# Kernel optimization log

Measured on AMD Instinct MI355X. Metric: run time of the kernel, lower is better.

The kernel has to match this reference:

```python
import jax, jax.numpy as jnp
import numpy as np

N = 50000
E = 800000
F_IN = 128
CONV_OUT = 128
CONV_LAYERS = 2
LSTM_OUT = 128
OUT_CH = 64


def setup_inputs() -> dict:
    key = jax.random.key(0)
    ks = jax.random.split(key, 16)
    s = 0.05
    inp = {
        "x": jax.random.normal(ks[0], (N, F_IN), jnp.float32),
        "edge_index": jax.random.randint(ks[1], (2, E), 0, N, dtype=jnp.int32),
        "edge_weight": jax.random.uniform(ks[2], (E,), jnp.float32),
        "H": jax.random.normal(ks[3], (1, N, LSTM_OUT), jnp.float32),
        "C": jax.random.normal(ks[4], (1, N, LSTM_OUT), jnp.float32),
        # GatedGraphConv params
        "ggc_weight": jax.random.normal(ks[5], (CONV_LAYERS, CONV_OUT, CONV_OUT), jnp.float32) * s,
        "gru_wih": jax.random.normal(ks[6], (3 * CONV_OUT, CONV_OUT), jnp.float32) * s,
        "gru_whh": jax.random.normal(ks[7], (3 * CONV_OUT, CONV_OUT), jnp.float32) * s,
        "gru_bih": jax.random.normal(ks[8], (3 * CONV_OUT,), jnp.float32) * s,
        "gru_bhh": jax.random.normal(ks[9], (3 * CONV_OUT,), jnp.float32) * s,
        # LSTM params (single layer, gate order i,f,g,o as in torch)
        "lstm_wih": jax.random.normal(ks[10], (4 * LSTM_OUT, CONV_OUT), jnp.float32) * s,
        "lstm_whh": jax.random.normal(ks[11], (4 * LSTM_OUT, LSTM_OUT), jnp.float32) * s,
        "lstm_bih": jax.random.normal(ks[12], (4 * LSTM_OUT,), jnp.float32) * s,
        "lstm_bhh": jax.random.normal(ks[13], (4 * LSTM_OUT,), jnp.float32) * s,
        # output linear
        "lin_w": jax.random.normal(ks[14], (OUT_CH, LSTM_OUT), jnp.float32) * s,
        "lin_b": jax.random.normal(ks[15], (OUT_CH,), jnp.float32) * s,
    }
    return inp


def reference(x, edge_index, edge_weight, H, C, ggc_weight, gru_wih, gru_whh,
              gru_bih, gru_bhh, lstm_wih, lstm_whh, lstm_bih, lstm_bhh, lin_w, lin_b):
    n = x.shape[0]
    out_dim = ggc_weight.shape[1]
    # GatedGraphConv: zero-pad input features up to out_dim if needed
    if x.shape[1] < out_dim:
        h = jnp.pad(x, ((0, 0), (0, out_dim - x.shape[1])))
    else:
        h = x
    src, dst = edge_index[0], edge_index[1]
    for i in range(ggc_weight.shape[0]):
        m = h @ ggc_weight[i]                      # [N, out]
        msg = m[src] * edge_weight[:, None]        # gather + weight, [E, out]
        agg = jax.ops.segment_sum(msg, dst, num_segments=n)  # scatter-add
        # GRUCell(input=agg, hidden=h)
        gi = agg @ gru_wih.T + gru_bih
        gh = h @ gru_whh.T + gru_bhh
        i_r, i_z, i_n = jnp.split(gi, 3, axis=-1)
        h_r, h_z, h_n = jnp.split(gh, 3, axis=-1)
        r = jax.nn.sigmoid(i_r + h_r)
        z = jax.nn.sigmoid(i_z + h_z)
        ncand = jnp.tanh(i_n + r * h_n)
        h = (1.0 - z) * ncand + z * h
    # single-timestep, single-layer LSTM (torch gate order i,f,g,o)
    hx, cx = H[0], C[0]
    gates = h @ lstm_wih.T + lstm_bih + hx @ lstm_whh.T + lstm_bhh
    ig, fg, gg, og = jnp.split(gates, 4, axis=-1)
    ig = jax.nn.sigmoid(ig)
    fg = jax.nn.sigmoid(fg)
    gg = jnp.tanh(gg)
    og = jax.nn.sigmoid(og)
    c_new = fg * cx + ig * gg
    h_new = og * jnp.tanh(c_new)
    out = jax.nn.relu(h_new) @ lin_w.T + lin_b     # relu then linear head
    return (out, h_new[None], c_new[None])
```

## Files before the change

### kernel.cpp

```cpp
#include <hip/hip_runtime.h>
#include <math.h>

#define N_NODES 50000
#define E_EDGES 800000
#define KD 128
#define NBLK_SCAN 196
#define RT_TILES 3125
#define CELL_RB 128
#define CELL_STRIDE (CELL_RB * 4)
#define CELL_BLOCKS 1024
#define NBUCKETS 196
#define FB_CHUNK 3125

typedef __attribute__((ext_vector_type(8))) short bf16x8;
typedef __attribute__((ext_vector_type(4))) float f32x4;

__device__ __forceinline__ float fsig(float x) { return 1.f / (1.f + __expf(-x)); }
__device__ __forceinline__ float ftanh(float x) { return 1.f - 2.f / (1.f + __expf(2.f * x)); }

__device__ __forceinline__ unsigned short f2bf(float f) {
    unsigned u = __float_as_uint(f);
    return (unsigned short)((u + 0x7FFFu + ((u >> 16) & 1u)) >> 16);
}
__device__ __forceinline__ float bf2f(unsigned short b) {
    return __uint_as_float(((unsigned)b) << 16);
}
__device__ __forceinline__ bf16x8 ldfrag(const unsigned short* p) {
    return *(const bf16x8*)(const void*)p;
}
__device__ __forceinline__ void stage_frag(const unsigned short* g, unsigned short* l) {
    __builtin_amdgcn_global_load_lds(
        (const __attribute__((address_space(1))) unsigned int*)g,
        (__attribute__((address_space(3))) unsigned int*)l, 16, 0, 0);
}
__device__ __forceinline__ void cell_decode(int id, int& x, int& y) {
    y = ((id >> 6) << 3) + (id & 7);
    x = (id >> 3) & 7;
}

#define PB_XH 12500
#define PB_W  12684
#define PB_F  13068
#define PB_CD 16193
__global__ __launch_bounds__(256) void prologue(
        const float* __restrict__ x, const float* __restrict__ H,
        const float* __restrict__ gru_whh, const float* __restrict__ lstm_wih,
        const float* __restrict__ lstm_whh, const float* __restrict__ lin_w,
        const float* __restrict__ ggc_w, const float* __restrict__ gru_wih,
        const int* __restrict__ ei,
        unsigned short* __restrict__ hb, unsigned short* __restrict__ Hxb,
        unsigned short* __restrict__ whhb, unsigned short* __restrict__ lwihb,
        unsigned short* __restrict__ lwhhb, unsigned short* __restrict__ linwb,
        unsigned short* __restrict__ WfT, int* __restrict__ deg) {
    const int b = blockIdx.x;
    if (b < PB_XH) {
        int t = b * 256 + threadIdx.x;
        const int n4 = N_NODES * KD / 4;
        const float* in; unsigned short* out; int idx;
        if (t < n4) { in = x; out = hb; idx = t; }
        else { in = H; out = Hxb; idx = t - n4; }
        float4 v = ((const float4*)in)[idx];
        ushort4 o;
        o.x = f2bf(v.x); o.y = f2bf(v.y); o.z = f2bf(v.z); o.w = f2bf(v.w);
        ((ushort4*)out)[idx] = o;
    } else if (b < PB_W) {
        int t = (b - PB_XH) * 256 + threadIdx.x;
        const float* in; unsigned short* out; int idx;
        if      (t < 12288)  { in = gru_whh;  out = whhb;  idx = t; }
        else if (t < 28672)  { in = lstm_wih; out = lwihb; idx = t - 12288; }
        else if (t < 45056)  { in = lstm_whh; out = lwhhb; idx = t - 28672; }
        else if (t < 47104)  { in = lin_w;    out = linwb; idx = t - 45056; }
        else return;
        float4 v = ((const float4*)in)[idx];
        ushort4 o;
        o.x = f2bf(v.x); o.y = f2bf(v.y); o.z = f2bf(v.z); o.w = f2bf(v.w);
        ((ushort4*)out)[idx] = o;
    } else if (b < PB_F) {
        int j = b - PB_W;
        __shared__ float wi[128];
        int k = threadIdx.x & 127;
        int l = threadIdx.x >> 7;
        if (threadIdx.x < 128) wi[k] = gru_wih[j * 128 + k];
        __syncthreads();
        const float* wg = ggc_w + l * 16384 + k * 128;
        float s = 0.f;
#pragma unroll 8
        for (int c = 0; c < 128; c += 4) {
            float4 a = *(const float4*)(wg + c);
            s += a.x * wi[c] + a.y * wi[c + 1] + a.z * wi[c + 2] + a.w * wi[c + 3];
        }
        WfT[((size_t)l * 384 + j) * 128 + k] = f2bf(s);
    } else {
        int e = (b - PB_F) * 256 + threadIdx.x;
        if (e < E_EDGES) atomicAdd(&deg[ei[E_EDGES + e]], 1);
    }
}

__global__ __launch_bounds__(256) void scan_p1(const int* __restrict__ deg,
                                               int* __restrict__ excl,
                                               int* __restrict__ bsum) {
    __shared__ int part[256];
    const int t = threadIdx.x;
    const int i = blockIdx.x * 256 + t;
    int v = (i < N_NODES) ? deg[i] : 0;
    part[t] = v;
    __syncthreads();
#pragma unroll
    for (int off = 1; off < 256; off <<= 1) {
        int u = (t >= off) ? part[t - off] : 0;
        __syncthreads();
        part[t] += u;
        __syncthreads();
    }
    if (i < N_NODES) excl[i] = part[t] - v;
    if (t == 255) bsum[blockIdx.x] = part[255];
}

__global__ __launch_bounds__(256) void scan_p2(int* __restrict__ bsum,
                                               int* __restrict__ rowptrN) {
    __shared__ int part[256];
    const int t = threadIdx.x;
    int v = (t < NBLK_SCAN) ? bsum[t] : 0;
    part[t] = v;
    __syncthreads();
#pragma unroll
    for (int off = 1; off < 256; off <<= 1) {
        int u = (t >= off) ? part[t - off] : 0;
        __syncthreads();
        part[t] += u;
        __syncthreads();
    }
    if (t < NBLK_SCAN) bsum[t] = part[t] - v;
    if (t == 255) *rowptrN = part[255];
}

__global__ __launch_bounds__(256) void scan_p3(const int* __restrict__ bsum,
                                               int* __restrict__ rowptr,
                                               int* __restrict__ bucketCur) {
    int i = blockIdx.x * 256 + threadIdx.x;
    if (i >= N_NODES) return;
    int r = rowptr[i] + bsum[blockIdx.x];
    rowptr[i] = r;
    if ((i & 255) == 0) bucketCur[i >> 8] = r;
}

__global__ __launch_bounds__(256) void fill_bucket(const int* __restrict__ ei,
                                                   const float* __restrict__ ew,
                                                   int* __restrict__ bucketCur,
                                                   int2* __restrict__ stage_sw,
                                                   int* __restrict__ stage_dst) {
    __shared__ int hist[NBUCKETS];
    __shared__ int base[NBUCKETS];
    __shared__ int loff[NBUCKETS];
    const int t = threadIdx.x;
    const int e0 = blockIdx.x * FB_CHUNK;
    const int e1 = min(e0 + FB_CHUNK, E_EDGES);
    for (int i = t; i < NBUCKETS; i += 256) { hist[i] = 0; loff[i] = 0; }
    __syncthreads();
    for (int e = e0 + t; e < e1; e += 256)
        atomicAdd(&hist[ei[E_EDGES + e] >> 8], 1);
    __syncthreads();
    for (int i = t; i < NBUCKETS; i += 256)
        base[i] = hist[i] ? atomicAdd(&bucketCur[i], hist[i]) : 0;
    __syncthreads();
    for (int e = e0 + t; e < e1; e += 256) {
        int dst = ei[E_EDGES + e];
        int bk = dst >> 8;
        int pos = base[bk] + atomicAdd(&loff[bk], 1);
        int2 pk;
        pk.x = ei[e];
        pk.y = __float_as_int(ew[e]);
        stage_sw[pos] = pk;
        stage_dst[pos] = dst;
    }
}

__global__ __launch_bounds__(256) void fill_final(const int* __restrict__ rowptr,
                                                  const int2* __restrict__ stage_sw,
                                                  const int* __restrict__ stage_dst,
                                                  int2* __restrict__ sEdge) {
    __shared__ int rbase[256];
    __shared__ int cnt[256];
    __shared__ int e1s;
    const int b = blockIdx.x;
    const int t = threadIdx.x;
    const int node0 = b << 8;
    const int nn = min(256, N_NODES - node0);
    if (t < nn) rbase[t] = rowptr[node0 + t];
    cnt[t] = 0;
    if (t == 0) e1s = rowptr[min(node0 + 256, N_NODES)];
    __syncthreads();
    const int e0 = rbase[0];
    const int e1 = e1s;
    for (int e = e0 + t; e < e1; e += 256) {
        int dl = stage_dst[e] & 255;
        int pos = rbase[dl] + atomicAdd(&cnt[dl], 1);
        sEdge[pos] = stage_sw[e];
    }
}

__global__ __launch_bounds__(256) void gather_agg_bf16(const unsigned short* __restrict__ m,
                                                       const int* __restrict__ rowptr,
                                                       const int2* __restrict__ sEdge,
                                                       unsigned short* __restrict__ agg) {
    int wid = (blockIdx.x * 256 + threadIdx.x) >> 6;
    if (wid >= N_NODES) return;
    int lane = threadIdx.x & 63;
    int q = lane >> 4, li = lane & 15;
    int f0 = li << 3;
    int e0 = rowptr[wid], e1 = rowptr[wid + 1];
    float acc[8] = {0.f, 0.f, 0.f, 0.f, 0.f, 0.f, 0.f, 0.f};
    int e = e0 + q;
    bf16x8 v = {0, 0, 0, 0, 0, 0, 0, 0};
    float w0 = 0.f;
    if (e < e1) {
        int2 pk0 = sEdge[e];
        w0 = __int_as_float(pk0.y);
        v = ldfrag(m + (size_t)pk0.x * KD + f0);
    }
    int2 pk1 = make_int2(0, 0);
    if (e + 4 < e1) pk1 = sEdge[e + 4];
    for (; e < e1; e += 4) {
        float wc = w0;
        bf16x8 vc = v;
        if (e + 4 < e1) {
            w0 = __int_as_float(pk1.y);
            v = ldfrag(m + (size_t)pk1.x * KD + f0);
        }
        if (e + 8 < e1) pk1 = sEdge[e + 8];
#pragma unroll
        for (int j = 0; j < 8; ++j)
            acc[j] += wc * bf2f((unsigned short)vc[j]);
    }
#pragma unroll
    for (int j = 0; j < 8; ++j) {
        acc[j] += __shfl_xor(acc[j], 16, 64);
        acc[j] += __shfl_xor(acc[j], 32, 64);
    }
    if (q == 0) {
        bf16x8 o;
#pragma unroll
        for (int j = 0; j < 8; ++j) o[j] = (short)f2bf(acc[j]);
        *(bf16x8*)(agg + (size_t)wid * KD + f0) = o;
    }
}

__global__ __launch_bounds__(256) void gru_fused(const unsigned short* __restrict__ Agg,
                                                 const unsigned short* __restrict__ Hin,
                                                 unsigned short* __restrict__ Hout,
                                                 const unsigned short* __restrict__ Wih,
                                                 const unsigned short* __restrict__ Whh,
                                                 const float* __restrict__ bih,
                                                 const float* __restrict__ bhh) {
    int cg, rb;
    cell_decode(blockIdx.x, cg, rb);
    __shared__ unsigned short lds[24 * 512];
    const int lane = threadIdx.x & 63, wave = threadIdx.x >> 6;
    const int rl = lane & 15, kg = lane >> 4;
    const int col0 = cg * 16;
    for (int q = wave; q < 24; q += 4) {
        int s = q >> 2, kk = q & 3;
        const unsigned short* src = (s < 3 ? Wih + (size_t)s * 128 * KD
                                           : Whh + (size_t)(s - 3) * 128 * KD)
                                    + (size_t)(col0 + rl) * KD + kk * 32 + kg * 8;
        stage_frag(src, lds + q * 512);
    }
    __syncthreads();
    const int col = col0 + rl;
    const float b_ir = bih[col], b_iz = bih[128 + col], b_in = bih[256 + col];
    const float b_hr = bhh[col], b_hz = bhh[128 + col], b_hn = bhh[256 + col];
    int rt = rb * 4 + wave;
    if (rt >= RT_TILES) return;
    bf16x8 a1[4], a2[4];
    unsigned short hvc[4];
#pragma unroll
    for (int kk = 0; kk < 4; ++kk) {
        a1[kk] = ldfrag(Agg + ((size_t)rt * 16 + rl) * KD + kk * 32 + kg * 8);
        a2[kk] = ldfrag(Hin + ((size_t)rt * 16 + rl) * KD + kk * 32 + kg * 8);
    }
#pragma unroll
    for (int p = 0; p < 4; ++p)
        hvc[p] = Hin[(size_t)(rt * 16 + kg * 4 + p) * KD + col];
    while (rt < RT_TILES) {
        const int rtn = rt + CELL_STRIDE;
        bf16x8 n1[4], n2[4];
        unsigned short hvn[4];
        if (rtn < RT_TILES) {
#pragma unroll
            for (int kk = 0; kk < 4; ++kk) {
                n1[kk] = ldfrag(Agg + ((size_t)rtn * 16 + rl) * KD + kk * 32 + kg * 8);
                n2[kk] = ldfrag(Hin + ((size_t)rtn * 16 + rl) * KD + kk * 32 + kg * 8);
            }
#pragma unroll
            for (int p = 0; p < 4; ++p)
                hvn[p] = Hin[(size_t)(rtn * 16 + kg * 4 + p) * KD + col];
        }
        f32x4 ir = {0.f,0.f,0.f,0.f}, iz = ir, in_ = ir, hr = ir, hz = ir, hn = ir;
#pragma unroll
        for (int kk = 0; kk < 4; ++kk) {
            ir  = __builtin_amdgcn_mfma_f32_16x16x32_bf16(a1[kk], ldfrag(lds + (0*4+kk)*512 + lane*8), ir,  0, 0, 0);
            iz  = __builtin_amdgcn_mfma_f32_16x16x32_bf16(a1[kk], ldfrag(lds + (1*4+kk)*512 + lane*8), iz,  0, 0, 0);
            in_ = __builtin_amdgcn_mfma_f32_16x16x32_bf16(a1[kk], ldfrag(lds + (2*4+kk)*512 + lane*8), in_, 0, 0, 0);
            hr  = __builtin_amdgcn_mfma_f32_16x16x32_bf16(a2[kk], ldfrag(lds + (3*4+kk)*512 + lane*8), hr,  0, 0, 0);
            hz  = __builtin_amdgcn_mfma_f32_16x16x32_bf16(a2[kk], ldfrag(lds + (4*4+kk)*512 + lane*8), hz,  0, 0, 0);
            hn  = __builtin_amdgcn_mfma_f32_16x16x32_bf16(a2[kk], ldfrag(lds + (5*4+kk)*512 + lane*8), hn,  0, 0, 0);
        }
#pragma unroll
        for (int p = 0; p < 4; ++p) {
            int row = rt * 16 + kg * 4 + p;
            float r = fsig(ir[p] + b_ir + hr[p] + b_hr);
            float z = fsig(iz[p] + b_iz + hz[p] + b_hz);
            float nc = ftanh(in_[p] + b_in + r * (hn[p] + b_hn));
            float hv = bf2f(hvc[p]);
            Hout[(size_t)row * KD + col] = f2bf((1.f - z) * nc + z * hv);
        }
        rt = rtn;
#pragma unroll
        for (int kk = 0; kk < 4; ++kk) { a1[kk] = n1[kk]; a2[kk] = n2[kk]; }
#pragma unroll
        for (int p = 0; p < 4; ++p) hvc[p] = hvn[p];
    }
}

__global__ __launch_bounds__(256) void lstm_fused(const unsigned short* __restrict__ Hh,
                                                  const unsigned short* __restrict__ Hx,
                                                  const float* __restrict__ Cx,
                                                  const unsigned short* __restrict__ Wih,
                                                  const unsigned short* __restrict__ Whh,
                                                  const float* __restrict__ bih,
                                                  const float* __restrict__ bhh,
                                                  float* __restrict__ h_out,
                                                  float* __restrict__ c_out,
                                                  unsigned short* __restrict__ Hrelu) {
    int cg, rb;
    cell_decode(blockIdx.x, cg, rb);
    __shared__ unsigned short lds[32 * 512];
    const int lane = threadIdx.x & 63, wave = threadIdx.x >> 6;
    const int rl = lane & 15, kg = lane >> 4;
    const int col0 = cg * 16;
    for (int q = wave; q < 32; q += 4) {
        int s = q >> 2, kk = q & 3;
        const unsigned short* src = (s < 4 ? Wih + (size_t)s * 128 * KD
                                           : Whh + (size_t)(s - 4) * 128 * KD)
                                    + (size_t)(col0 + rl) * KD + kk * 32 + kg * 8;
        stage_frag(src, lds + q * 512);
    }
    __syncthreads();
    const int col = col0 + rl;
    const float b_i = bih[col] + bhh[col];
    const float b_f = bih[128 + col] + bhh[128 + col];
    const float b_g = bih[256 + col] + bhh[256 + col];
    const float b_o = bih[384 + col] + bhh[384 + col];
    int rt = rb * 4 + wave;
    if (rt >= RT_TILES) return;
    bf16x8 a1[4], a2[4];
    float cpre[4];
#pragma unroll
    for (int kk = 0; kk < 4; ++kk) {
        a1[kk] = ldfrag(Hh + ((size_t)rt * 16 + rl) * KD + kk * 32 + kg * 8);
        a2[kk] = ldfrag(Hx + ((size_t)rt * 16 + rl) * KD + kk * 32 + kg * 8);
    }
#pragma unroll
    for (int p = 0; p < 4; ++p)
        cpre[p] = Cx[(size_t)(rt * 16 + kg * 4 + p) * KD + col];
    while (rt < RT_TILES) {
        const int rtn = rt + CELL_STRIDE;
        bf16x8 n1[4], n2[4];
        float cnx[4];
        if (rtn < RT_TILES) {
#pragma unroll
            for (int kk = 0; kk < 4; ++kk) {
                n1[kk] = ldfrag(Hh + ((size_t)rtn * 16 + rl) * KD + kk * 32 + kg * 8);
                n2[kk] = ldfrag(Hx + ((size_t)rtn * 16 + rl) * KD + kk * 32 + kg * 8);
            }
#pragma unroll
            for (int p = 0; p < 4; ++p)
                cnx[p] = Cx[(size_t)(rtn * 16 + kg * 4 + p) * KD + col];
        }
        f32x4 gi = {0.f,0.f,0.f,0.f}, gf = gi, gg = gi, go = gi;
        f32x4 hi = gi, hf = gi, hg = gi, ho = gi;
#pragma unroll
        for (int kk = 0; kk < 4; ++kk) {
            gi = __builtin_amdgcn_mfma_f32_16x16x32_bf16(a1[kk], ldfrag(lds + (0*4+kk)*512 + lane*8), gi, 0, 0, 0);
            gf = __builtin_amdgcn_mfma_f32_16x16x32_bf16(a1[kk], ldfrag(lds + (1*4+kk)*512 + lane*8), gf, 0, 0, 0);
            gg = __builtin_amdgcn_mfma_f32_16x16x32_bf16(a1[kk], ldfrag(lds + (2*4+kk)*512 + lane*8), gg, 0, 0, 0);
            go = __builtin_amdgcn_mfma_f32_16x16x32_bf16(a1[kk], ldfrag(lds + (3*4+kk)*512 + lane*8), go, 0, 0, 0);
            hi = __builtin_amdgcn_mfma_f32_16x16x32_bf16(a2[kk], ldfrag(lds + (4*4+kk)*512 + lane*8), hi, 0, 0, 0);
            hf = __builtin_amdgcn_mfma_f32_16x16x32_bf16(a2[kk], ldfrag(lds + (5*4+kk)*512 + lane*8), hf, 0, 0, 0);
            hg = __builtin_amdgcn_mfma_f32_16x16x32_bf16(a2[kk], ldfrag(lds + (6*4+kk)*512 + lane*8), hg, 0, 0, 0);
            ho = __builtin_amdgcn_mfma_f32_16x16x32_bf16(a2[kk], ldfrag(lds + (7*4+kk)*512 + lane*8), ho, 0, 0, 0);
        }
#pragma unroll
        for (int p = 0; p < 4; ++p) {
            int row = rt * 16 + kg * 4 + p;
            size_t idx = (size_t)row * KD + col;
            float ig = fsig(gi[p] + hi[p] + b_i);
            float fg = fsig(gf[p] + hf[p] + b_f);
            float gv = ftanh(gg[p] + hg[p] + b_g);
            float og = fsig(go[p] + ho[p] + b_o);
            float c = fg * cpre[p] + ig * gv;
            float hn = og * ftanh(c);
            c_out[idx] = c;
            h_out[idx] = hn;
            Hrelu[idx] = f2bf(fmaxf(hn, 0.f));
        }
        rt = rtn;
#pragma unroll
        for (int kk = 0; kk < 4; ++kk) { a1[kk] = n1[kk]; a2[kk] = n2[kk]; }
#pragma unroll
        for (int p = 0; p < 4; ++p) cpre[p] = cnx[p];
    }
}

__global__ __launch_bounds__(256) void head_gemm(const unsigned short* __restrict__ Hr,
                                                 const unsigned short* __restrict__ LinW,
                                                 const float* __restrict__ lin_b,
                                                 float* __restrict__ Out) {
    __shared__ unsigned short wlds[16 * 512];
    const int lane = threadIdx.x & 63, wave = threadIdx.x >> 6;
    const int rl = lane & 15, kg = lane >> 4;
    for (int f = wave; f < 16; f += 4) {
        int jt = f >> 2, kk = f & 3;
        stage_frag(LinW + (size_t)(jt * 16 + rl) * KD + kk * 32 + kg * 8, wlds + f * 512);
    }
    __syncthreads();
    const int stride = gridDim.x << 2;
    int rt = blockIdx.x * 4 + wave;
    if (rt >= RT_TILES) return;
    bf16x8 a[4];
#pragma unroll
    for (int kk = 0; kk < 4; ++kk)
        a[kk] = ldfrag(Hr + ((size_t)rt * 16 + rl) * KD + kk * 32 + kg * 8);
    while (rt < RT_TILES) {
        const int rtn = rt + stride;
        bf16x8 an[4];
        if (rtn < RT_TILES) {
#pragma unroll
            for (int kk = 0; kk < 4; ++kk)
                an[kk] = ldfrag(Hr + ((size_t)rtn * 16 + rl) * KD + kk * 32 + kg * 8);
        }
#pragma unroll
        for (int jt = 0; jt < 4; ++jt) {
            f32x4 acc = {0.f, 0.f, 0.f, 0.f};
#pragma unroll
            for (int kk = 0; kk < 4; ++kk)
                acc = __builtin_amdgcn_mfma_f32_16x16x32_bf16(
                    a[kk], ldfrag(wlds + (jt * 4 + kk) * 512 + lane * 8), acc, 0, 0, 0);
            int col = jt * 16 + rl;
            float b = lin_b[col];
#pragma unroll
            for (int p = 0; p < 4; ++p)
                Out[(size_t)(rt * 16 + kg * 4 + p) * 64 + col] = acc[p] + b;
        }
        rt = rtn;
#pragma unroll
        for (int kk = 0; kk < 4; ++kk) a[kk] = an[kk];
    }
}

extern "C" void kernel_launch(void* const* d_in, const int* in_sizes, int n_in,
                              void* d_out, int out_size, void* d_ws, size_t ws_size,
                              hipStream_t stream) {
    const float* x        = (const float*)d_in[0];
    const int*   ei       = (const int*)d_in[1];
    const float* ew       = (const float*)d_in[2];
    const float* H        = (const float*)d_in[3];
    const float* C        = (const float*)d_in[4];
    const float* ggc_w    = (const float*)d_in[5];
    const float* gru_wih  = (const float*)d_in[6];
    const float* gru_whh  = (const float*)d_in[7];
    const float* gru_bih  = (const float*)d_in[8];
    const float* gru_bhh  = (const float*)d_in[9];
    const float* lstm_wih = (const float*)d_in[10];
    const float* lstm_whh = (const float*)d_in[11];
    const float* lstm_bih = (const float*)d_in[12];
    const float* lstm_bhh = (const float*)d_in[13];
    const float* lin_w    = (const float*)d_in[14];
    const float* lin_b    = (const float*)d_in[15];

    float* out_head = (float*)d_out;
    float* h_out = out_head + (size_t)N_NODES * 64;
    float* c_out = h_out + (size_t)N_NODES * KD;

    char* w = (char*)d_ws;
    unsigned short* hb    = (unsigned short*)w; w += (size_t)N_NODES * KD * 2;
    unsigned short* hb1   = (unsigned short*)w; w += (size_t)N_NODES * KD * 2;
    unsigned short* Hxb   = (unsigned short*)w; w += (size_t)N_NODES * KD * 2;
    unsigned short* mb    = (unsigned short*)w; w += (size_t)N_NODES * KD * 2;
    unsigned short* aggb  = (unsigned short*)w; w += (size_t)N_NODES * KD * 2;
    unsigned short* WfT   = (unsigned short*)w; w += 2 * 384 * KD * 2;
    unsigned short* whhb  = (unsigned short*)w; w += 384 * KD * 2;
    unsigned short* lwihb = (unsigned short*)w; w += 512 * KD * 2;
    unsigned short* lwhhb = (unsigned short*)w; w += 512 * KD * 2;
    unsigned short* linwb = (unsigned short*)w; w += 64 * KD * 2;
    int*   rowptr    = (int*)w; w += 50304 * 4;
    int*   deg       = (int*)w; w += 50304 * 4;
    int*   bsum      = (int*)w; w += 256 * 4;
    int*   bucketCur = (int*)w; w += 256 * 4;
    int2*  sEdge     = (int2*)w; w += (size_t)E_EDGES * 8;
    int2*  stage_sw  = (int2*)w; w += (size_t)E_EDGES * 8;
    int*   stage_dst = (int*)w; w += (size_t)E_EDGES * 4;

    dim3 blk(256);

    hipMemsetAsync(deg, 0, N_NODES * sizeof(int), stream);
    prologue<<<PB_CD, blk, 0, stream>>>(x, H, gru_whh, lstm_wih, lstm_whh, lin_w,
                                        ggc_w, gru_wih, ei,
                                        hb, Hxb, whhb, lwihb, lwhhb, linwb, WfT, deg);
    scan_p1<<<NBLK_SCAN, blk, 0, stream>>>(deg, rowptr, bsum);
    scan_p2<<<1, blk, 0, stream>>>(bsum, rowptr + N_NODES);
    scan_p3<<<NBLK_SCAN, blk, 0, stream>>>(bsum, rowptr, bucketCur);
    fill_bucket<<<256, blk, 0, stream>>>(ei, ew, bucketCur, stage_sw, stage_dst);
    fill_final<<<NBUCKETS, blk, 0, stream>>>(rowptr, stage_sw, stage_dst, sEdge);

    gather_agg_bf16<<<(N_NODES * 64 + 255) / 256, blk, 0, stream>>>(
        hb, rowptr, sEdge, aggb);
    gru_fused<<<CELL_BLOCKS, blk, 0, stream>>>(aggb, hb, hb1,
                                               WfT, whhb, gru_bih, gru_bhh);
    gather_agg_bf16<<<(N_NODES * 64 + 255) / 256, blk, 0, stream>>>(
        hb1, rowptr, sEdge, aggb);
    gru_fused<<<CELL_BLOCKS, blk, 0, stream>>>(aggb, hb1, hb,
                                               WfT + (size_t)384 * KD, whhb, gru_bih, gru_bhh);

    lstm_fused<<<CELL_BLOCKS, blk, 0, stream>>>(hb, Hxb, C, lwihb, lwhhb,
                                                lstm_bih, lstm_bhh, h_out, c_out, mb);
    head_gemm<<<391, blk, 0, stream>>>(mb, linwb, lin_b, out_head);
}
```

Measured before the change: 270.6 us.

## Build CSR from per-bucket histograms instead of a global per-node degree scan

The per-node global-atomic degree count and three-kernel scan are replaced with a shared-memory bucket histogram folded into the prologue and a single-block scan over 196 buckets. Per-node row pointers are then computed inside fill_final through a local count and block scan within each bucket. This removes 800K global atomics, a 50K-element memset and two kernel launches. In exchange, fill_final reads stage_dst twice and runs an extra block-level scan.

```diff
diff --git a/kernel.cpp b/kernel.cpp
--- a/kernel.cpp
+++ b/kernel.cpp
@@ -4,7 +4,6 @@
 #define N_NODES 50000
 #define E_EDGES 800000
 #define KD 128
-#define NBLK_SCAN 196
 #define RT_TILES 3125
 #define CELL_RB 128
 #define CELL_STRIDE (CELL_RB * 4)
@@ -41,7 +40,7 @@
 #define PB_XH 12500
 #define PB_W  12684
 #define PB_F  13068
-#define PB_CD 16193
+#define PB_TOT 13324
 __global__ __launch_bounds__(256) void prologue(
         const float* __restrict__ x, const float* __restrict__ H,
         const float* __restrict__ gru_whh, const float* __restrict__ lstm_wih,
@@ -51,7 +50,7 @@
         unsigned short* __restrict__ hb, unsigned short* __restrict__ Hxb,
         unsigned short* __restrict__ whhb, unsigned short* __restrict__ lwihb,
         unsigned short* __restrict__ lwhhb, unsigned short* __restrict__ linwb,
-        unsigned short* __restrict__ WfT, int* __restrict__ deg) {
+        unsigned short* __restrict__ WfT, int* __restrict__ bucketTotal) {
     const int b = blockIdx.x;
     if (b < PB_XH) {
         int t = b * 256 + threadIdx.x;
@@ -91,18 +90,26 @@
         }
         WfT[((size_t)l * 384 + j) * 128 + k] = f2bf(s);
     } else {
-        int e = (b - PB_F) * 256 + threadIdx.x;
-        if (e < E_EDGES) atomicAdd(&deg[ei[E_EDGES + e]], 1);
-    }
-}
-
-__global__ __launch_bounds__(256) void scan_p1(const int* __restrict__ deg,
-                                               int* __restrict__ excl,
-                                               int* __restrict__ bsum) {
+        __shared__ int hist[NBUCKETS];
+        const int t = threadIdx.x;
+        const int e0 = (b - PB_F) * FB_CHUNK;
+        const int e1 = min(e0 + FB_CHUNK, E_EDGES);
+        for (int i = t; i < NBUCKETS; i += 256) hist[i] = 0;
+        __syncthreads();
+        for (int e = e0 + t; e < e1; e += 256)
+            atomicAdd(&hist[ei[E_EDGES + e] >> 8], 1);
+        __syncthreads();
+        for (int i = t; i < NBUCKETS; i += 256)
+            if (hist[i]) atomicAdd(&bucketTotal[i], hist[i]);
+    }
+}
+
+__global__ __launch_bounds__(256) void scan_buckets(const int* __restrict__ bucketTotal,
+                                                    int* __restrict__ bucketBase,
+                                                    int* __restrict__ bucketCur) {
     __shared__ int part[256];
     const int t = threadIdx.x;
-    const int i = blockIdx.x * 256 + t;
-    int v = (i < N_NODES) ? deg[i] : 0;
+    int v = (t < NBUCKETS) ? bucketTotal[t] : 0;
     part[t] = v;
     __syncthreads();
 #pragma unroll
@@ -112,36 +119,12 @@
         part[t] += u;
         __syncthreads();
     }
-    if (i < N_NODES) excl[i] = part[t] - v;
-    if (t == 255) bsum[blockIdx.x] = part[255];
-}
-
-__global__ __launch_bounds__(256) void scan_p2(int* __restrict__ bsum,
-                                               int* __restrict__ rowptrN) {
-    __shared__ int part[256];
-    const int t = threadIdx.x;
-    int v = (t < NBLK_SCAN) ? bsum[t] : 0;
-    part[t] = v;
-    __syncthreads();
-#pragma unroll
-    for (int off = 1; off < 256; off <<= 1) {
-        int u = (t >= off) ? part[t - off] : 0;
-        __syncthreads();
-        part[t] += u;
-        __syncthreads();
-    }
-    if (t < NBLK_SCAN) bsum[t] = part[t] - v;
-    if (t == 255) *rowptrN = part[255];
-}
-
-__global__ __launch_bounds__(256) void scan_p3(const int* __restrict__ bsum,
-                                               int* __restrict__ rowptr,
-                                               int* __restrict__ bucketCur) {
-    int i = blockIdx.x * 256 + threadIdx.x;
-    if (i >= N_NODES) return;
-    int r = rowptr[i] + bsum[blockIdx.x];
-    rowptr[i] = r;
-    if ((i & 255) == 0) bucketCur[i >> 8] = r;
+    if (t < NBUCKETS) {
+        int base = part[t] - v;
+        bucketBase[t] = base;
+        bucketCur[t] = base;
+    }
+    if (t == NBUCKETS - 1) bucketBase[NBUCKETS] = part[t];
 }
 
 __global__ __launch_bounds__(256) void fill_bucket(const int* __restrict__ ei,
@@ -175,26 +158,41 @@
     }
 }
 
-__global__ __launch_bounds__(256) void fill_final(const int* __restrict__ rowptr,
+__global__ __launch_bounds__(256) void fill_final(const int* __restrict__ bucketBase,
                                                   const int2* __restrict__ stage_sw,
                                                   const int* __restrict__ stage_dst,
-                                                  int2* __restrict__ sEdge) {
-    __shared__ int rbase[256];
+                                                  int2* __restrict__ sEdge,
+                                                  int* __restrict__ rowptr) {
     __shared__ int cnt[256];
-    __shared__ int e1s;
+    __shared__ int off[256];
     const int b = blockIdx.x;
     const int t = threadIdx.x;
     const int node0 = b << 8;
-    const int nn = min(256, N_NODES - node0);
-    if (t < nn) rbase[t] = rowptr[node0 + t];
+    const int e0 = bucketBase[b];
+    const int e1 = bucketBase[b + 1];
     cnt[t] = 0;
-    if (t == 0) e1s = rowptr[min(node0 + 256, N_NODES)];
-    __syncthreads();
-    const int e0 = rbase[0];
-    const int e1 = e1s;
+    __syncthreads();
+    for (int e = e0 + t; e < e1; e += 256)
+        atomicAdd(&cnt[stage_dst[e] & 255], 1);
+    __syncthreads();
+    int v = cnt[t];
+    off[t] = v;
+    __syncthreads();
+#pragma unroll
+    for (int o = 1; o < 256; o <<= 1) {
+        int u = (t >= o) ? off[t - o] : 0;
+        __syncthreads();
+        off[t] += u;
+        __syncthreads();
+    }
+    const int excl = off[t] - v;
+    if (node0 + t < N_NODES) rowptr[node0 + t] = e0 + excl;
+    if (b == NBUCKETS - 1 && t == 0) rowptr[N_NODES] = e1;
+    cnt[t] = excl;
+    __syncthreads();
     for (int e = e0 + t; e < e1; e += 256) {
         int dl = stage_dst[e] & 255;
-        int pos = rbase[dl] + atomicAdd(&cnt[dl], 1);
+        int pos = e0 + atomicAdd(&cnt[dl], 1);
         sEdge[pos] = stage_sw[e];
     }
 }
@@ -493,25 +491,25 @@
     unsigned short* lwihb = (unsigned short*)w; w += 512 * KD * 2;
     unsigned short* lwhhb = (unsigned short*)w; w += 512 * KD * 2;
     unsigned short* linwb = (unsigned short*)w; w += 64 * KD * 2;
-    int*   rowptr    = (int*)w; w += 50304 * 4;
-    int*   deg       = (int*)w; w += 50304 * 4;
-    int*   bsum      = (int*)w; w += 256 * 4;
-    int*   bucketCur = (int*)w; w += 256 * 4;
-    int2*  sEdge     = (int2*)w; w += (size_t)E_EDGES * 8;
-    int2*  stage_sw  = (int2*)w; w += (size_t)E_EDGES * 8;
-    int*   stage_dst = (int*)w; w += (size_t)E_EDGES * 4;
+    int*   rowptr      = (int*)w; w += 50304 * 4;
+    int*   bucketTotal = (int*)w; w += 256 * 4;
+    int*   bucketBase  = (int*)w; w += 256 * 4;
+    int*   bucketCur   = (int*)w; w += 256 * 4;
+    int2*  sEdge       = (int2*)w; w += (size_t)E_EDGES * 8;
+    int2*  stage_sw    = (int2*)w; w += (size_t)E_EDGES * 8;
+    int*   stage_dst   = (int*)w; w += (size_t)E_EDGES * 4;
 
     dim3 blk(256);
 
-    hipMemsetAsync(deg, 0, N_NODES * sizeof(int), stream);
-    prologue<<<PB_CD, blk, 0, stream>>>(x, H, gru_whh, lstm_wih, lstm_whh, lin_w,
-                                        ggc_w, gru_wih, ei,
-                                        hb, Hxb, whhb, lwihb, lwhhb, linwb, WfT, deg);
-    scan_p1<<<NBLK_SCAN, blk, 0, stream>>>(deg, rowptr, bsum);
-    scan_p2<<<1, blk, 0, stream>>>(bsum, rowptr + N_NODES);
-    scan_p3<<<NBLK_SCAN, blk, 0, stream>>>(bsum, rowptr, bucketCur);
+    hipMemsetAsync(bucketTotal, 0, NBUCKETS * sizeof(int), stream);
+    prologue<<<PB_TOT, blk, 0, stream>>>(x, H, gru_whh, lstm_wih, lstm_whh, lin_w,
+                                         ggc_w, gru_wih, ei,
+                                         hb, Hxb, whhb, lwihb, lwhhb, linwb, WfT,
+                                         bucketTotal);
+    scan_buckets<<<1, blk, 0, stream>>>(bucketTotal, bucketBase, bucketCur);
     fill_bucket<<<256, blk, 0, stream>>>(ei, ew, bucketCur, stage_sw, stage_dst);
-    fill_final<<<NBUCKETS, blk, 0, stream>>>(rowptr, stage_sw, stage_dst, sEdge);
+    fill_final<<<NBUCKETS, blk, 0, stream>>>(bucketBase, stage_sw, stage_dst,
+                                             sEdge, rowptr);
 
     gather_agg_bf16<<<(N_NODES * 64 + 255) / 256, blk, 0, stream>>>(
         hb, rowptr, sEdge, aggb);
```

New measurement: 266.5 us, median of 2. Within noise of the previous version (-1.5%).
